# Optimization experiments

Measured on AMD Instinct MI355X. Metric: run time of the kernel, lower is better.

Reference implementation:

```python
import jax, jax.numpy as jnp
import numpy as np

# Model hyperparameters (upscaled from the repo's shakespear config)
L, E, H, T, B, V = 6, 1024, 16, 1024, 4, 32000
HD = E // H          # head_size = 64
EPS = 1e-5


def layernorm(x, g, b):
    m = x.mean(-1, keepdims=True)
    v = ((x - m) ** 2).mean(-1, keepdims=True)
    return (x - m) / jnp.sqrt(v + EPS) * g + b


def setup_inputs() -> dict:
    key = jax.random.key(0)
    ks = jax.random.split(key, 24)
    s = 0.02
    n = lambda k, shp: (jax.random.normal(k, shp) * s).astype(jnp.float32)
    return {
        "idx": jax.random.randint(ks[0], (B, T), 0, V),
        "tok_emb": n(ks[1], (V, E)),
        "pos_emb": n(ks[2], (T, E)),
        # per-head q/k/v weights stacked: [L, E, H, HD]
        "Wq": n(ks[3], (L, E, H, HD)),
        "Wk": n(ks[4], (L, E, H, HD)),
        "Wv": n(ks[5], (L, E, H, HD)),
        "Wo": n(ks[6], (L, E, E)),
        "bo": jnp.zeros((L, E), jnp.float32),
        "W1": n(ks[7], (L, E, 4 * E)),
        "b1": jnp.zeros((L, 4 * E), jnp.float32),
        "W2": n(ks[8], (L, 4 * E, E)),
        "b2": jnp.zeros((L, E), jnp.float32),
        "ln1_g": jnp.ones((L, E), jnp.float32),
        "ln1_b": jnp.zeros((L, E), jnp.float32),
        "ln2_g": jnp.ones((L, E), jnp.float32),
        "ln2_b": jnp.zeros((L, E), jnp.float32),
        "lnf_g": jnp.ones((E,), jnp.float32),
        "lnf_b": jnp.zeros((E,), jnp.float32),
        "Wlm": n(ks[9], (E, V)),
        "blm": jnp.zeros((V,), jnp.float32),
    }


def reference(idx, tok_emb, pos_emb, Wq, Wk, Wv, Wo, bo, W1, b1, W2, b2,
              ln1_g, ln1_b, ln2_g, ln2_b, lnf_g, lnf_b, Wlm, blm):
    x = tok_emb[idx] + pos_emb[None, :T]            # [B,T,E]
    mask = jnp.tril(jnp.ones((T, T), bool))
    scale = HD ** -0.5
    for l in range(L):
        h = layernorm(x, ln1_g[l], ln1_b[l])
        q = jnp.einsum('bte,ehd->bhtd', h, Wq[l])
        k = jnp.einsum('bte,ehd->bhtd', h, Wk[l])
        v = jnp.einsum('bte,ehd->bhtd', h, Wv[l])
        # NOTE: source computes K @ Q^T (reversed from standard attention)
        wei = jnp.einsum('bhtd,bhsd->bhts', k, q) * scale
        wei = jnp.where(mask, wei, -jnp.inf)
        wei = jax.nn.softmax(wei, axis=-1)
        att = jnp.einsum('bhts,bhsd->bhtd', wei, v)  # [B,H,T,HD]
        att = att.transpose(0, 2, 1, 3).reshape(B, T, E)
        x = x + att @ Wo[l] + bo[l]
        h2 = layernorm(x, ln2_g[l], ln2_b[l])
        x = x + jax.nn.relu(h2 @ W1[l] + b1[l]) @ W2[l] + b2[l]
    x = layernorm(x, lnf_g, lnf_b)
    logits = x @ Wlm + blm                           # [B,T,V]
    return logits
```

## Files before the change

kernel.cpp:

```cpp
#include <hip/hip_runtime.h>


typedef __bf16 bf16;
typedef __attribute__((ext_vector_type(8))) __bf16 bf16x8;
typedef __attribute__((ext_vector_type(4))) __bf16 bf16x4;
typedef __attribute__((ext_vector_type(4))) float  f32x4;

#define LAYERS 6
#define EMB    1024
#define HEADS  16
#define HDIM   64
#define SEQ    1024
#define BATCH  4
#define VOCAB  32000
#define ROWS   (BATCH * SEQ)

#define AS1(p) ((__attribute__((address_space(1))) void*)(p))
#define AS3(p) ((__attribute__((address_space(3))) void*)(p))

__global__ void transpose_cvt(const float* __restrict__ in, bf16* __restrict__ out,
                              int K, int N)
{
    __shared__ float tile[32][33];
    int n0 = blockIdx.x * 32, k0 = blockIdx.y * 32;
    int tx = threadIdx.x, ty = threadIdx.y;
#pragma unroll
    for (int r = 0; r < 4; ++r)
        tile[ty + 8 * r][tx] = in[(size_t)(k0 + ty + 8 * r) * N + n0 + tx];
    __syncthreads();
#pragma unroll
    for (int r = 0; r < 4; ++r)
        out[(size_t)(n0 + ty + 8 * r) * K + k0 + tx] = (bf16)tile[tx][ty + 8 * r];
}

__global__ void transpose4_cvt(const float* __restrict__ s0, const float* __restrict__ s1,
                               const float* __restrict__ s2, const float* __restrict__ s3,
                               bf16* __restrict__ d0, bf16* __restrict__ d1,
                               bf16* __restrict__ d2, bf16* __restrict__ d3)
{
    const float* in; bf16* out;
    switch (blockIdx.z) {
        case 0: in = s0; out = d0; break;
        case 1: in = s1; out = d1; break;
        case 2: in = s2; out = d2; break;
        default: in = s3; out = d3; break;
    }
    __shared__ float tile[32][33];
    int n0 = blockIdx.x * 32, k0 = blockIdx.y * 32;
    int tx = threadIdx.x, ty = threadIdx.y;
#pragma unroll
    for (int r = 0; r < 4; ++r)
        tile[ty + 8 * r][tx] = in[(size_t)(k0 + ty + 8 * r) * 1024 + n0 + tx];
    __syncthreads();
#pragma unroll
    for (int r = 0; r < 4; ++r)
        out[(size_t)(n0 + ty + 8 * r) * 1024 + k0 + tx] = (bf16)tile[tx][ty + 8 * r];
}

__global__ void embed_kernel(const int* __restrict__ idx, const float* __restrict__ tok,
                             const float* __restrict__ pos, float* __restrict__ x)
{
    int row = blockIdx.x;
    int t   = row & (SEQ - 1);
    int id  = idx[row];
    int e   = threadIdx.x;
    float4 a = ((const float4*)(tok + (size_t)id * EMB))[e];
    float4 p = ((const float4*)(pos + (size_t)t  * EMB))[e];
    float4 r; r.x = a.x + p.x; r.y = a.y + p.y; r.z = a.z + p.z; r.w = a.w + p.w;
    ((float4*)(x + (size_t)row * EMB))[e] = r;
}

__global__ __launch_bounds__(256)
void ln_kernel(const float* __restrict__ x, const float* __restrict__ g,
               const float* __restrict__ b, bf16* __restrict__ out)
{
    int row = blockIdx.x;
    int t = threadIdx.x;
    float4 v = ((const float4*)(x + (size_t)row * EMB))[t];
    float s1 = v.x + v.y + v.z + v.w;
    float s2 = v.x * v.x + v.y * v.y + v.z * v.z + v.w * v.w;
#pragma unroll
    for (int off = 32; off > 0; off >>= 1) {
        s1 += __shfl_down(s1, off);
        s2 += __shfl_down(s2, off);
    }
    __shared__ float l1[4], l2[4];
    int wave = t >> 6;
    if ((t & 63) == 0) { l1[wave] = s1; l2[wave] = s2; }
    __syncthreads();
    float tot1 = l1[0] + l1[1] + l1[2] + l1[3];
    float tot2 = l2[0] + l2[1] + l2[2] + l2[3];
    float mean = tot1 * (1.f / EMB);
    float var  = tot2 * (1.f / EMB) - mean * mean;
    float rstd = rsqrtf(var + 1e-5f);
    float4 gg = ((const float4*)g)[t];
    float4 bb = ((const float4*)b)[t];
    bf16x4 o;
    o.x = (bf16)((v.x - mean) * rstd * gg.x + bb.x);
    o.y = (bf16)((v.y - mean) * rstd * gg.y + bb.y);
    o.z = (bf16)((v.z - mean) * rstd * gg.z + bb.z);
    o.w = (bf16)((v.w - mean) * rstd * gg.w + bb.w);
    *(bf16x4*)(out + (size_t)row * EMB + t * 4) = o;
}

template <int MODE>
__global__ __launch_bounds__(512, 1)
void gemm256_kernel(const bf16* __restrict__ A, const bf16* __restrict__ BT,
                    void* Cv, const float* __restrict__ bias,
                    int N, int K, int nbm, int nbn)
{
    __shared__ __align__(16) bf16 lds[2][2][256 * 64];
    const int tid  = threadIdx.x;
    const int wave = tid >> 6, lane = tid & 63;
    const int lo = lane & 15, hi = lane >> 4;
    const int wm = wave >> 2, wn = wave & 3;

    const int nwg = nbm * nbn;
    const int q = nwg >> 3, rem = nwg & 7;
    const int xcd = blockIdx.x & 7, boff = blockIdx.x >> 3;
    const int swz = (xcd < rem ? xcd * (q + 1) : rem * (q + 1) + (xcd - rem) * q) + boff;
    const int m0 = (swz % nbm) * 256;
    const int n0 = (swz / nbm) * 256;

    f32x4 acc[8][4];
#pragma unroll
    for (int m = 0; m < 8; ++m)
#pragma unroll
        for (int n = 0; n < 4; ++n)
            acc[m][n] = (f32x4){0.f, 0.f, 0.f, 0.f};

    const int NT = K >> 6;

    auto stage_ht = [&](int t, int ht) {
        const int slot = t & 1;
        const int k0 = t << 6;
        const int ab = ht >> 1;
        const int rbase = (ht & 1) << 7;
        const bf16* src = ab ? BT : A;
        const int base0 = ab ? n0 : m0;
#pragma unroll
        for (int j = 0; j < 2; ++j) {
            int g  = j * 512 + tid;
            int r  = g >> 3;
            int cc = (g & 7) ^ (r & 7);
            __builtin_amdgcn_global_load_lds(
                AS1(src + (size_t)(base0 + rbase + r) * K + k0 + cc * 8),
                AS3((char*)&lds[slot][ab][rbase * 64] + (size_t)g * 16), 16, 0, 0);
        }
    };

    bf16x8 bcur[4][2], bnxt[4][2], ae[2][2], ao[2][2];

    auto lda = [&](int t, int mp, bf16x8 (&out)[2][2]) {
        const int slot = t & 1;
#pragma unroll
        for (int mi = 0; mi < 2; ++mi)
#pragma unroll
            for (int ks = 0; ks < 2; ++ks) {
                int r = wm * 128 + (mp * 2 + mi) * 16 + lo;
                int pos = (ks * 4 + hi) ^ (r & 7);
                out[mi][ks] = *(const bf16x8*)(&lds[slot][0][r * 64 + pos * 8]);
            }
    };
    auto ldb = [&](int t, bf16x8 (&out)[4][2]) {
        const int slot = t & 1;
#pragma unroll
        for (int n = 0; n < 4; ++n)
#pragma unroll
            for (int ks = 0; ks < 2; ++ks) {
                int r = wn * 64 + n * 16 + lo;
                int pos = (ks * 4 + hi) ^ (r & 7);
                out[n][ks] = *(const bf16x8*)(&lds[slot][1][r * 64 + pos * 8]);
            }
    };
    auto mfma16 = [&](int mp, bf16x8 (&a)[2][2]) {
        __builtin_amdgcn_s_setprio(1);
#pragma unroll
        for (int mi = 0; mi < 2; ++mi)
#pragma unroll
            for (int n = 0; n < 4; ++n)
#pragma unroll
                for (int ks = 0; ks < 2; ++ks)
                    acc[mp * 2 + mi][n] =
                        __builtin_amdgcn_mfma_f32_16x16x32_bf16(a[mi][ks], bcur[n][ks],
                                                                acc[mp * 2 + mi][n], 0, 0, 0);
        __builtin_amdgcn_s_setprio(0);
    };

    stage_ht(0, 0); stage_ht(0, 1); stage_ht(0, 2); stage_ht(0, 3);
    asm volatile("s_waitcnt vmcnt(0)\n\ts_barrier" ::: "memory");
    ldb(0, bcur);
    lda(0, 0, ae);

    for (int t = 0; t < NT; ++t) {
        const bool more = (t + 1 < NT);
        if (more) { stage_ht(t + 1, 0); stage_ht(t + 1, 1); }
        lda(t, 1, ao);
        mfma16(0, ae);
        if (more) { stage_ht(t + 1, 2); stage_ht(t + 1, 3); }
        lda(t, 2, ae);
        mfma16(1, ao);
        lda(t, 3, ao);
        mfma16(2, ae);
        if (more) {
            asm volatile("s_waitcnt vmcnt(0) lgkmcnt(0)\n\ts_barrier" ::: "memory");
            ldb(t + 1, bnxt);
            lda(t + 1, 0, ae);
        }
        mfma16(3, ao);
        if (more) {
#pragma unroll
            for (int n = 0; n < 4; ++n)
#pragma unroll
                for (int ks = 0; ks < 2; ++ks)
                    bcur[n][ks] = bnxt[n][ks];
        }
    }

#pragma unroll
    for (int m = 0; m < 8; ++m) {
        int row = m0 + wm * 128 + m * 16 + hi * 4;
#pragma unroll
        for (int n = 0; n < 4; ++n) {
            int col = n0 + wn * 64 + n * 16 + lo;
            float bv = (MODE != 0) ? bias[col] : 0.f;
#pragma unroll
            for (int j = 0; j < 4; ++j) {
                size_t o = (size_t)(row + j) * N + col;
                float v = acc[m][n][j] + bv;
                if (MODE == 2)      ((bf16*)Cv)[o]  = (bf16)fmaxf(v, 0.f);
                else if (MODE == 3) ((float*)Cv)[o] = v;
                else                ((bf16*)Cv)[o]  = (bf16)v;
            }
        }
    }
}

template <int MODE>
__global__ __launch_bounds__(256)
void gemm_kernel(const bf16* __restrict__ A, const bf16* __restrict__ BT,
                 void* Cv, const float* __restrict__ bias,
                 const float* resid, int N, int K)
{
    __shared__ __align__(16) bf16 As[128 * 64];
    __shared__ __align__(16) bf16 Bs[128 * 64];
    const int tid = threadIdx.x;
    const int wave = tid >> 6, lane = tid & 63;
    const int lo = lane & 15, hi = lane >> 4;
    const int wm = wave >> 1, wn = wave & 1;
    const int m0 = blockIdx.y * 128, n0 = blockIdx.x * 128;

    f32x4 acc[4][4];
#pragma unroll
    for (int m = 0; m < 4; ++m)
#pragma unroll
        for (int n = 0; n < 4; ++n)
            acc[m][n] = (f32x4){0.f, 0.f, 0.f, 0.f};

    const int sb = wave * 4;
    for (int k0 = 0; k0 < K; k0 += 64) {
#pragma unroll
        for (int i = 0; i < 4; ++i) {
            int g   = (sb + i) * 64 + lane;
            int row = g >> 3;
            int lc  = (g & 7) ^ (row & 7);
            const bf16* ga = A  + (size_t)(m0 + row) * K + k0 + lc * 8;
            const bf16* gb = BT + (size_t)(n0 + row) * K + k0 + lc * 8;
            __builtin_amdgcn_global_load_lds(AS1(ga), AS3(As + (sb + i) * 512), 16, 0, 0);
            __builtin_amdgcn_global_load_lds(AS1(gb), AS3(Bs + (sb + i) * 512), 16, 0, 0);
        }
        asm volatile("s_waitcnt vmcnt(0)" ::: "memory");
        __syncthreads();
#pragma unroll
        for (int ks = 0; ks < 2; ++ks) {
            bf16x8 af[4], bfr[4];
#pragma unroll
            for (int m = 0; m < 4; ++m) {
                int r  = wm * 64 + m * 16 + lo;
                int pc = (ks * 4 + hi) ^ (r & 7);
                af[m] = *(const bf16x8*)(As + r * 64 + pc * 8);
            }
#pragma unroll
            for (int n = 0; n < 4; ++n) {
                int r  = wn * 64 + n * 16 + lo;
                int pc = (ks * 4 + hi) ^ (r & 7);
                bfr[n] = *(const bf16x8*)(Bs + r * 64 + pc * 8);
            }
#pragma unroll
            for (int m = 0; m < 4; ++m)
#pragma unroll
                for (int n = 0; n < 4; ++n)
                    acc[m][n] = __builtin_amdgcn_mfma_f32_16x16x32_bf16(af[m], bfr[n], acc[m][n], 0, 0, 0);
        }
        __syncthreads();
    }

#pragma unroll
    for (int m = 0; m < 4; ++m) {
        int rbase = m0 + wm * 64 + m * 16 + hi * 4;
#pragma unroll
        for (int n = 0; n < 4; ++n) {
            int col = n0 + wn * 64 + n * 16 + lo;
            float bv = (MODE != 0) ? bias[col] : 0.f;
#pragma unroll
            for (int j = 0; j < 4; ++j) {
                size_t off = (size_t)(rbase + j) * N + col;
                float v = acc[m][n][j] + bv;
                if (MODE == 1)      ((float*)Cv)[off] = v + resid[off];
                else if (MODE == 2) ((bf16*)Cv)[off]  = (bf16)fmaxf(v, 0.f);
                else if (MODE == 3) ((float*)Cv)[off] = v;
                else                ((bf16*)Cv)[off]  = (bf16)v;
            }
        }
    }
}

__global__ void vtrans_kernel(const bf16* __restrict__ qkv, bf16* __restrict__ vt)
{
    int bh = blockIdx.x; int b = bh >> 4, h = bh & 15;
    int t0 = blockIdx.y * 64;
    __shared__ bf16 tile[64][68];
    int tx = threadIdx.x, ty = threadIdx.y;
#pragma unroll
    for (int r = 0; r < 16; ++r) {
        int t = r * 4 + ty;
        tile[t][tx] = qkv[(size_t)(b * SEQ + t0 + t) * 3072 + 2048 + h * 64 + tx];
    }
    __syncthreads();
#pragma unroll
    for (int r = 0; r < 16; ++r) {
        int d = r * 4 + ty;
        vt[((size_t)bh * 64 + d) * SEQ + t0 + tx] = tile[tx][d];
    }
}

__global__ __launch_bounds__(64)
void attn_kernel(const bf16* __restrict__ qkv, const bf16* __restrict__ vt,
                 bf16* __restrict__ att)
{
    int bh = blockIdx.x; int b = bh >> 4, h = bh & 15;
    int t0 = blockIdx.y * 16;
    int lane = threadIdx.x;
    int lo = lane & 15, hi = lane >> 4;
    const bf16* kb = qkv + (size_t)(b * SEQ) * 3072 + EMB + h * 64;
    const bf16* qb = qkv + (size_t)(b * SEQ) * 3072 + h * 64;
    const bf16* vb = vt + (size_t)bh * 64 * SEQ;

    bf16x8 bK0 = *(const bf16x8*)(kb + (size_t)(t0 + lo) * 3072 + hi * 8);
    bf16x8 bK1 = *(const bf16x8*)(kb + (size_t)(t0 + lo) * 3072 + 32 + hi * 8);

    f32x4 o[4];
#pragma unroll
    for (int n = 0; n < 4; ++n) o[n] = (f32x4){0.f, 0.f, 0.f, 0.f};
    float mrun = -1e30f, lrun = 0.f;

    __shared__ __align__(16) bf16 plds[16][72];

    const int nt = (t0 + 16 + 63) >> 6;
    const int nfull = (t0 >= 64) ? (((t0 - 63) >> 6) + 1) : 0;

    auto tile_body = [&](int s0, bool masked) {
        f32x4 sc[4];
#pragma unroll
        for (int sh = 0; sh < 4; ++sh) sc[sh] = (f32x4){0.f, 0.f, 0.f, 0.f};
#pragma unroll
        for (int sh = 0; sh < 4; ++sh) {
            const bf16* qr = qb + (size_t)(s0 + sh * 16 + lo) * 3072;
            bf16x8 aQ0 = *(const bf16x8*)(qr + hi * 8);
            bf16x8 aQ1 = *(const bf16x8*)(qr + 32 + hi * 8);
            sc[sh] = __builtin_amdgcn_mfma_f32_16x16x32_bf16(aQ0, bK0, sc[sh], 0, 0, 0);
            sc[sh] = __builtin_amdgcn_mfma_f32_16x16x32_bf16(aQ1, bK1, sc[sh], 0, 0, 0);
        }
        const int tt = t0 + lo;
        float p[16];
        float mx = -1e30f;
#pragma unroll
        for (int sh = 0; sh < 4; ++sh)
#pragma unroll
            for (int j = 0; j < 4; ++j) {
                float val = sc[sh][j] * 0.125f;
                if (masked) {
                    int s = s0 + sh * 16 + hi * 4 + j;
                    if (s > tt) val = -1e30f;
                }
                p[sh * 4 + j] = val;
                mx = fmaxf(mx, val);
            }
        mx = fmaxf(mx, __shfl_xor(mx, 16));
        mx = fmaxf(mx, __shfl_xor(mx, 32));
        float mnew = fmaxf(mrun, mx);
        float scl = __expf(mrun - mnew);
        mrun = mnew;
        float rs = 0.f;
#pragma unroll
        for (int i = 0; i < 16; ++i) { p[i] = __expf(p[i] - mnew); rs += p[i]; }
        rs += __shfl_xor(rs, 16);
        rs += __shfl_xor(rs, 32);
        lrun = lrun * scl + rs;
        float sclj[4];
#pragma unroll
        for (int j = 0; j < 4; ++j) sclj[j] = __shfl(scl, hi * 4 + j);
#pragma unroll
        for (int n = 0; n < 4; ++n)
#pragma unroll
            for (int j = 0; j < 4; ++j)
                o[n][j] *= sclj[j];
        __syncthreads();
#pragma unroll
        for (int sh = 0; sh < 4; ++sh) {
            bf16x4 w;
            w.x = (bf16)p[sh * 4 + 0]; w.y = (bf16)p[sh * 4 + 1];
            w.z = (bf16)p[sh * 4 + 2]; w.w = (bf16)p[sh * 4 + 3];
            *(bf16x4*)(&plds[lo][sh * 16 + hi * 4]) = w;
        }
        __syncthreads();
        bf16x8 aP0 = *(const bf16x8*)(&plds[lo][hi * 8]);
        bf16x8 aP1 = *(const bf16x8*)(&plds[lo][32 + hi * 8]);
#pragma unroll
        for (int n = 0; n < 4; ++n) {
            bf16x8 bV0 = *(const bf16x8*)(vb + (size_t)(n * 16 + lo) * SEQ + s0 + hi * 8);
            bf16x8 bV1 = *(const bf16x8*)(vb + (size_t)(n * 16 + lo) * SEQ + s0 + 32 + hi * 8);
            o[n] = __builtin_amdgcn_mfma_f32_16x16x32_bf16(aP0, bV0, o[n], 0, 0, 0);
            o[n] = __builtin_amdgcn_mfma_f32_16x16x32_bf16(aP1, bV1, o[n], 0, 0, 0);
        }
    };

    for (int it = 0; it < nfull; ++it) tile_body(it * 64, false);
    for (int it = nfull; it < nt; ++it) tile_body(it * 64, true);

    float lj[4];
#pragma unroll
    for (int j = 0; j < 4; ++j) lj[j] = __shfl(lrun, hi * 4 + j);
#pragma unroll
    for (int j = 0; j < 4; ++j) {
        float inv = 1.f / lj[j];
        size_t rowoff = (size_t)(b * SEQ + t0 + hi * 4 + j) * EMB + h * 64;
#pragma unroll
        for (int n = 0; n < 4; ++n)
            att[rowoff + n * 16 + lo] = (bf16)(o[n][j] * inv);
    }
}

extern "C" void kernel_launch(void* const* d_in, const int* in_sizes, int n_in,
                              void* d_out, int out_size, void* d_ws, size_t ws_size,
                              hipStream_t stream)
{
    const int*   idx  = (const int*)d_in[0];
    const float* tok  = (const float*)d_in[1];
    const float* pos  = (const float*)d_in[2];
    const float* Wq   = (const float*)d_in[3];
    const float* Wk   = (const float*)d_in[4];
    const float* Wv   = (const float*)d_in[5];
    const float* Wo   = (const float*)d_in[6];
    const float* bo   = (const float*)d_in[7];
    const float* W1   = (const float*)d_in[8];
    const float* b1   = (const float*)d_in[9];
    const float* W2   = (const float*)d_in[10];
    const float* b2   = (const float*)d_in[11];
    const float* ln1g = (const float*)d_in[12];
    const float* ln1b = (const float*)d_in[13];
    const float* ln2g = (const float*)d_in[14];
    const float* ln2b = (const float*)d_in[15];
    const float* lnfg = (const float*)d_in[16];
    const float* lnfb = (const float*)d_in[17];
    const float* Wlm  = (const float*)d_in[18];
    const float* blm  = (const float*)d_in[19];
    float* out = (float*)d_out;

    char* ws = (char*)d_ws;
    size_t off = 0;
    auto alloc = [&](size_t bytes) { void* p = ws + off; off += (bytes + 255) & ~(size_t)255; return p; };
    float* x    = (float*)alloc((size_t)ROWS * EMB * 4);
    bf16* h     = (bf16*)alloc((size_t)ROWS * EMB * 2);
    bf16* qkv   = (bf16*)alloc((size_t)ROWS * 3072 * 2);
    bf16* vt    = (bf16*)alloc((size_t)ROWS * EMB * 2);
    bf16* attb  = (bf16*)alloc((size_t)ROWS * EMB * 2);
    bf16* mlp   = (bf16*)alloc((size_t)ROWS * 4096 * 2);
    bf16* WTqkv = (bf16*)alloc((size_t)3072 * 1024 * 2);
    bf16* WTo   = (bf16*)alloc((size_t)1024 * 1024 * 2);
    bf16* WT1   = (bf16*)alloc((size_t)4096 * 1024 * 2);
    bf16* WT2   = (bf16*)alloc((size_t)1024 * 4096 * 2);
    bf16* WTlm  = (bf16*)alloc((size_t)VOCAB * 1024 * 2);

    dim3 tb(32, 8);

    transpose_cvt<<<dim3(VOCAB / 32, 32), tb, 0, stream>>>(Wlm, WTlm, 1024, VOCAB);

    embed_kernel<<<ROWS, 256, 0, stream>>>(idx, tok, pos, x);

    for (int l = 0; l < LAYERS; ++l) {
        const size_t wqs = (size_t)l * 1024 * 1024;
        const size_t w14 = (size_t)l * 4096 * 1024;
        transpose4_cvt<<<dim3(32, 32, 4), tb, 0, stream>>>(
            Wq + wqs, Wk + wqs, Wv + wqs, Wo + wqs,
            WTqkv, WTqkv + (size_t)1024 * 1024, WTqkv + (size_t)2048 * 1024, WTo);
        transpose_cvt<<<dim3(128, 32), tb, 0, stream>>>(W1 + w14, WT1, 1024, 4096);
        transpose_cvt<<<dim3(32, 128), tb, 0, stream>>>(W2 + w14, WT2, 4096, 1024);

        ln_kernel<<<ROWS, 256, 0, stream>>>(x, ln1g + l * EMB, ln1b + l * EMB, h);
        gemm256_kernel<0><<<16 * 12, 512, 0, stream>>>(h, WTqkv, qkv, nullptr, 3072, 1024, 16, 12);
        vtrans_kernel<<<dim3(64, 16), dim3(64, 4), 0, stream>>>(qkv, vt);
        attn_kernel<<<dim3(64, 64), 64, 0, stream>>>(qkv, vt, attb);
        gemm_kernel<1><<<dim3(8, 32), 256, 0, stream>>>(attb, WTo, x, bo + l * EMB, x, 1024, 1024);
        ln_kernel<<<ROWS, 256, 0, stream>>>(x, ln2g + l * EMB, ln2b + l * EMB, h);
        gemm256_kernel<2><<<16 * 16, 512, 0, stream>>>(h, WT1, mlp, b1 + l * 4096, 4096, 1024, 16, 16);
        gemm_kernel<1><<<dim3(8, 32), 256, 0, stream>>>(mlp, WT2, x, b2 + l * EMB, x, 1024, 4096);
    }
    ln_kernel<<<ROWS, 256, 0, stream>>>(x, lnfg, lnfb, h);
    gemm256_kernel<3><<<16 * 125, 512, 0, stream>>>(h, WTlm, out, blm, 32000, 1024, 16, 125);
}
```

Measured before the change: 2.141 ms.

## Store residual stream in bf16 and merge W1/W2 transposes into one launch

Switches the residual activation buffer x from fp32 to bf16 across the embedding, layernorm and residual-add GEMM epilogues, halving the bytes read and written for the residual stream. It also fuses the separate W1 and W2 weight transpose-convert launches into one kernel that uses the z grid dimension. Keeping the residual in bf16 accumulates rounding error over six layers, which may push the output past the accuracy tolerance.

```diff
diff --git a/kernel.cpp b/kernel.cpp
--- a/kernel.cpp
+++ b/kernel.cpp
@@ -57,8 +57,27 @@
         out[(size_t)(n0 + ty + 8 * r) * 1024 + k0 + tx] = (bf16)tile[tx][ty + 8 * r];
 }
 
+__global__ void transpose_w12(const float* __restrict__ W1, const float* __restrict__ W2,
+                              bf16* __restrict__ T1, bf16* __restrict__ T2)
+{
+    __shared__ float tile[32][33];
+    int tx = threadIdx.x, ty = threadIdx.y;
+    const float* in; bf16* out; int K, N, n0, k0;
+    if (blockIdx.z == 0) { in = W1; out = T1; K = 1024; N = 4096;
+                           n0 = blockIdx.x * 32; k0 = blockIdx.y * 32; }
+    else                 { in = W2; out = T2; K = 4096; N = 1024;
+                           n0 = blockIdx.y * 32; k0 = blockIdx.x * 32; }
+#pragma unroll
+    for (int r = 0; r < 4; ++r)
+        tile[ty + 8 * r][tx] = in[(size_t)(k0 + ty + 8 * r) * N + n0 + tx];
+    __syncthreads();
+#pragma unroll
+    for (int r = 0; r < 4; ++r)
+        out[(size_t)(n0 + ty + 8 * r) * K + k0 + tx] = (bf16)tile[tx][ty + 8 * r];
+}
+
 __global__ void embed_kernel(const int* __restrict__ idx, const float* __restrict__ tok,
-                             const float* __restrict__ pos, float* __restrict__ x)
+                             const float* __restrict__ pos, bf16* __restrict__ x)
 {
     int row = blockIdx.x;
     int t   = row & (SEQ - 1);
@@ -66,17 +85,20 @@
     int e   = threadIdx.x;
     float4 a = ((const float4*)(tok + (size_t)id * EMB))[e];
     float4 p = ((const float4*)(pos + (size_t)t  * EMB))[e];
-    float4 r; r.x = a.x + p.x; r.y = a.y + p.y; r.z = a.z + p.z; r.w = a.w + p.w;
-    ((float4*)(x + (size_t)row * EMB))[e] = r;
+    bf16x4 o;
+    o.x = (bf16)(a.x + p.x); o.y = (bf16)(a.y + p.y);
+    o.z = (bf16)(a.z + p.z); o.w = (bf16)(a.w + p.w);
+    *(bf16x4*)(x + (size_t)row * EMB + e * 4) = o;
 }
 
 __global__ __launch_bounds__(256)
-void ln_kernel(const float* __restrict__ x, const float* __restrict__ g,
+void ln_kernel(const bf16* __restrict__ x, const float* __restrict__ g,
                const float* __restrict__ b, bf16* __restrict__ out)
 {
     int row = blockIdx.x;
     int t = threadIdx.x;
-    float4 v = ((const float4*)(x + (size_t)row * EMB))[t];
+    bf16x4 xv = *(const bf16x4*)(x + (size_t)row * EMB + t * 4);
+    float4 v; v.x = (float)xv.x; v.y = (float)xv.y; v.z = (float)xv.z; v.w = (float)xv.w;
     float s1 = v.x + v.y + v.z + v.w;
     float s2 = v.x * v.x + v.y * v.y + v.z * v.z + v.w * v.w;
 #pragma unroll
@@ -240,7 +262,7 @@
 __global__ __launch_bounds__(256)
 void gemm_kernel(const bf16* __restrict__ A, const bf16* __restrict__ BT,
                  void* Cv, const float* __restrict__ bias,
-                 const float* resid, int N, int K)
+                 const bf16* __restrict__ resid, int N, int K)
 {
     __shared__ __align__(16) bf16 As[128 * 64];
     __shared__ __align__(16) bf16 Bs[128 * 64];
@@ -306,8 +328,8 @@
             for (int j = 0; j < 4; ++j) {
                 size_t off = (size_t)(rbase + j) * N + col;
                 float v = acc[m][n][j] + bv;
-                if (MODE == 1)      ((float*)Cv)[off] = v + resid[off];
-                else if (MODE == 2) ((bf16*)Cv)[off]  = (bf16)fmaxf(v, 0.f);
+                if (MODE == 1)      ((bf16*)Cv)[off] = (bf16)(v + (float)resid[off]);
+                else if (MODE == 2) ((bf16*)Cv)[off] = (bf16)fmaxf(v, 0.f);
                 else if (MODE == 3) ((float*)Cv)[off] = v;
                 else                ((bf16*)Cv)[off]  = (bf16)v;
             }
@@ -470,7 +492,7 @@
     char* ws = (char*)d_ws;
     size_t off = 0;
     auto alloc = [&](size_t bytes) { void* p = ws + off; off += (bytes + 255) & ~(size_t)255; return p; };
-    float* x    = (float*)alloc((size_t)ROWS * EMB * 4);
+    bf16* x     = (bf16*)alloc((size_t)ROWS * EMB * 2);
     bf16* h     = (bf16*)alloc((size_t)ROWS * EMB * 2);
     bf16* qkv   = (bf16*)alloc((size_t)ROWS * 3072 * 2);
     bf16* vt    = (bf16*)alloc((size_t)ROWS * EMB * 2);
@@ -494,8 +516,7 @@
         transpose4_cvt<<<dim3(32, 32, 4), tb, 0, stream>>>(
             Wq + wqs, Wk + wqs, Wv + wqs, Wo + wqs,
             WTqkv, WTqkv + (size_t)1024 * 1024, WTqkv + (size_t)2048 * 1024, WTo);
-        transpose_cvt<<<dim3(128, 32), tb, 0, stream>>>(W1 + w14, WT1, 1024, 4096);
-        transpose_cvt<<<dim3(32, 128), tb, 0, stream>>>(W2 + w14, WT2, 4096, 1024);
+        transpose_w12<<<dim3(128, 32, 2), tb, 0, stream>>>(W1 + w14, W2 + w14, WT1, WT2);
 
         ln_kernel<<<ROWS, 256, 0, stream>>>(x, ln1g + l * EMB, ln1b + l * EMB, h);
         gemm256_kernel<0><<<16 * 12, 512, 0, stream>>>(h, WTqkv, qkv, nullptr, 3072, 1024, 16, 12);
```

Result: faster. 2.094 ms (-2.2%).
